# Kernel optimization log

Hardware: AMD Instinct MI355X
Metric: run time of the kernel (lower is better)

The kernel has to match this reference:

```python
import jax, jax.numpy as jnp
import numpy as np

_SQRT1_2 = 0.7071067811865476

B, S, D, N, NCH = 4, 2048, 1024, 32768, 8


def setup_inputs() -> dict:
    key = jax.random.key(0)
    ks = jax.random.split(key, 6)
    return {
        "x": jax.random.normal(ks[0], (B, S, D), jnp.float32),
        "h": jax.random.normal(ks[1], (B, S, D), jnp.float32),
        "emb": jax.random.normal(ks[2], (N, D), jnp.float32),
        "tau_offset": jax.random.normal(ks[3], (B, S, 1), jnp.float32),
        "w_read": jax.random.normal(ks[4], (N, D), jnp.float32),
        "w_write": jax.random.normal(ks[5], (N, D), jnp.float32),
        "n_chunks": NCH,
    }


def _srw_chunked(x, h, emb_unit, tau_offset, w_read, w_write, n_chunks):
    b, s, d = x.shape
    n = emb_unit.shape[0]
    cs = n // n_chunks
    h_bf = h.astype(jnp.bfloat16)
    x_bf = x.astype(jnp.bfloat16)
    emb_bf = emb_unit.astype(jnp.bfloat16)
    read_bf = w_read.astype(jnp.bfloat16)
    write_bf = w_write.astype(jnp.bfloat16)
    z1 = jnp.zeros((b, s, 1), jnp.float32)

    # ---- pass 1: online score statistics over chunks of N ----
    @jax.checkpoint
    def stats_step(carry, i):
        s_sum, sq_sum, cube_sum, ns_sum, ns_sq = carry
        ec = jax.lax.dynamic_slice_in_dim(emb_bf, i * cs, cs, axis=0)
        sc = (h_bf @ ec.T).astype(jnp.float32)  # [B,S,cs]
        s_sum = s_sum + sc.sum(-1, keepdims=True)
        sq_sum = sq_sum + (sc ** 2).sum(-1, keepdims=True)
        cube_sum = cube_sum + (sc ** 3).sum(-1, keepdims=True)
        pns = sc.mean(axis=(0, 1))  # per-neuron mean score [cs]
        return ((s_sum, sq_sum, cube_sum, ns_sum + pns.sum(), ns_sq + (pns ** 2).sum()), None)

    (s_sum, sq_sum, cube_sum, ns_sum, ns_sq), _ = jax.lax.scan(
        stats_step, (z1, z1, z1, jnp.float32(0.0), jnp.float32(0.0)), jnp.arange(n_chunks))

    s_mean = s_sum / n
    s_std = jnp.sqrt(sq_sum / n - s_mean ** 2) + 1e-08
    tau = s_mean + tau_offset * s_std
    cube_mean = cube_sum / n
    central_third = cube_mean - 3.0 * s_mean * s_std ** 2 - s_mean ** 3
    score_skew = jax.lax.stop_gradient((central_third / (s_std ** 3 + 1e-08)).mean())
    mean_score = ns_sum / n
    var_score = ns_sq / n - mean_score ** 2
    score_lb = var_score / (mean_score ** 2 + var_score + 0.01)

    # ---- pass 2: erf-threshold gate + read/write GEMM accumulate ----
    @jax.checkpoint
    def gate_step(carry, i):
        out, wcost, gmax, act, strong, phib, zsum, z075c, z030c, glg = carry
        s0 = i * cs
        ec = jax.lax.dynamic_slice_in_dim(emb_bf, s0, cs, axis=0)
        rc = jax.lax.dynamic_slice_in_dim(read_bf, s0, cs, axis=0)
        wc = jax.lax.dynamic_slice_in_dim(write_bf, s0, cs, axis=0)
        rc = rc / (jnp.linalg.norm(rc, axis=-1, keepdims=True) + 1e-08)
        wc = wc / (jnp.linalg.norm(wc, axis=-1, keepdims=True) + 1e-08)
        z = ((h_bf @ ec.T).astype(jnp.float32) - tau) / s_std  # [B,S,cs]
        phi = 0.5 * (1.0 + jax.lax.erf(z * _SQRT1_2))
        gate = jnp.where(z > 0, z * phi, 0.0)
        xr = x_bf @ rc.T  # [B,S,cs]
        c_out = ((gate.astype(jnp.bfloat16) * xr) @ wc).astype(jnp.float32)  # [B,S,D]
        g_safe = gate + 1e-08
        new = (
            out + c_out,
            wcost + gate.sum(-1, keepdims=True),
            jnp.maximum(gmax, gate.max(-1, keepdims=True)),
            act + (gate > 0.0).astype(jnp.float32).sum(-1, keepdims=True),
            strong + (gate > 0.5).astype(jnp.float32).sum(-1, keepdims=True),
            phib + ((phi > 0.95) | (phi < 0.05)).astype(jnp.float32).sum(-1, keepdims=True),
            zsum + jnp.where(z > 0, z, 0.0).sum(-1, keepdims=True),
            z075c + ((z > 0) & (z < 0.75)).astype(jnp.float32).sum(-1, keepdims=True),
            z030c + ((z > 0) & (z < 0.3)).astype(jnp.float32).sum(-1, keepdims=True),
            glg + (gate * jnp.log(g_safe)).sum(-1, keepdims=True),
        )
        return (new, None)

    init = (jnp.zeros((b, s, d), jnp.float32), z1, jnp.full((b, s, 1), -1e9, jnp.float32),
            z1, z1, z1, z1, z1, z1, z1)
    (raw_out, wcost, gmax, act, strong, phib, zsum, z075c, z030c, glg), _ = jax.lax.scan(
        gate_step, init, jnp.arange(n_chunks))

    den = jnp.maximum(wcost, 1.0)
    out = (raw_out / den).astype(jnp.bfloat16)
    score_std_out = s_std.mean()
    es_out = wcost.mean()
    active_n_mean = act.mean()
    z_mean_active = zsum / (act + 1e-08)
    active_eps = act + 1e-08
    z_lt_075_frac = jax.lax.stop_gradient((z075c / active_eps).mean())
    z_lt_030_frac = jax.lax.stop_gradient((z030c / active_eps).mean())
    tau_abs_mean = jax.lax.stop_gradient(tau).mean()
    active_per_token_std = jax.lax.stop_gradient(act).std()
    gate_sum_eps = wcost + 1e-08
    entropy_per_token = -glg / gate_sum_eps + jnp.log(gate_sum_eps)
    gate_entropy = jax.lax.stop_gradient(entropy_per_token).mean()
    return (out.astype(jnp.float32), act / n, gmax, score_lb, score_std_out, es_out,
            active_n_mean, strong / n, phib / n, z_mean_active, tau_abs_mean,
            z_lt_075_frac, z_lt_030_frac, score_skew, active_per_token_std, gate_entropy)


def reference(x, h, emb, tau_offset, w_read, w_write, n_chunks):
    emb_unit = emb / (jnp.linalg.norm(emb, axis=-1, keepdims=True) + 1e-08)
    return _srw_chunked(x, h, emb_unit, tau_offset, w_read, w_write, n_chunks)
```

## Files before the change

### kernel.cpp

```cpp
#include <hip/hip_runtime.h>

#define DEV __device__ __forceinline__

typedef __attribute__((ext_vector_type(4))) float f32x4;
typedef __attribute__((ext_vector_type(8))) short s16x8;
typedef __attribute__((ext_vector_type(8))) unsigned short u16x8;

static const int NTOK = 8192;
static const int DD   = 1024;
static const int NNEU = 32768;
static const int NC   = 8192;

static const int OUT_ACT    = 8388608;
static const int OUT_GMAX   = 8396800;
static const int OUT_SLB    = 8404992;
static const int OUT_SSTD   = 8404993;
static const int OUT_ES     = 8404994;
static const int OUT_ANM    = 8404995;
static const int OUT_STRONG = 8404996;
static const int OUT_PHIB   = 8413188;
static const int OUT_ZMEAN  = 8421380;
static const int OUT_TAUM   = 8429572;
static const int OUT_Z75    = 8429573;
static const int OUT_Z30    = 8429574;
static const int OUT_SKEW   = 8429575;
static const int OUT_ASTD   = 8429576;
static const int OUT_ENT    = 8429577;

DEV unsigned short f2bf(float f){
  unsigned u = __float_as_uint(f);
  u += 0x7fffu + ((u >> 16) & 1u);
  return (unsigned short)(u >> 16);
}
DEV float bf2f(unsigned short h){ return __uint_as_float(((unsigned)h) << 16); }
DEV float rnd_bf(float f){ return bf2f(f2bf(f)); }

template<int AUX>
DEV void gl_lds16(const void* g, void* l){
  __builtin_amdgcn_global_load_lds(
      (const __attribute__((address_space(1))) unsigned int*)g,
      (__attribute__((address_space(3))) unsigned int*)l, 16, 0, AUX);
}

DEV f32x4 mfma16(s16x8 a, s16x8 b, f32x4 c){
  return __builtin_amdgcn_mfma_f32_16x16x32_bf16(a, b, c, 0, 0, 0);
}

template<int AUX>
DEV void stage4(const unsigned short* __restrict__ G, size_t ld, int k0,
                unsigned short* L, int t){
  #pragma unroll
  for (int i = 0; i < 4; i++){
    int ch = i*256 + t;
    int row = ch >> 3, c = ch & 7;
    int cs = c ^ (row & 7);
    int wb = (i*256 + (t & 192)) * 16;
    gl_lds16<AUX>(G + (size_t)row * ld + k0 + cs*8, (char*)L + wb);
  }
}

DEV s16x8 frg(const unsigned short* L, int R, int kk, int lq){
  int cc = ((kk >> 3) + lq) ^ (R & 7);
  return *(const s16x8*)((const char*)L + R*128 + cc*16);
}

DEV void waitv_bar(){
  asm volatile("s_waitcnt vmcnt(0)" ::: "memory");
  __builtin_amdgcn_s_barrier();
  __builtin_amdgcn_sched_barrier(0);
}

DEV int2 xcd64(){
  int orig = blockIdx.y * 64 + blockIdx.x;
  int xcd = orig & 7, p = orig >> 3;
  int sqy = p >> 6, off = p & 63;
  int2 r;
  r.x = xcd*8 + (off & 7);
  r.y = sqy*8 + (off >> 3);
  return r;
}


__global__ __launch_bounds__(256) void k_norms(const float* __restrict__ e,
    const float* __restrict__ r_, const float* __restrict__ w_,
    float* __restrict__ inv_e, float* __restrict__ inv_r, float* __restrict__ inv_w){
  int t = threadIdx.x, l = t & 63, wv = t >> 6;
  int row = blockIdx.x * 4 + wv;
  const float4* ep = (const float4*)(e  + (size_t)row * DD);
  const float4* rp = (const float4*)(r_ + (size_t)row * DD);
  const float4* wp = (const float4*)(w_ + (size_t)row * DD);
  float se = 0.f, sr = 0.f, sw = 0.f;
  #pragma unroll
  for (int j = 0; j < 4; j++){
    float4 v = ep[j*64 + l];
    se += v.x*v.x + v.y*v.y + v.z*v.z + v.w*v.w;
    float4 a = rp[j*64 + l];
    float a0 = rnd_bf(a.x), a1 = rnd_bf(a.y), a2 = rnd_bf(a.z), a3 = rnd_bf(a.w);
    sr += a0*a0 + a1*a1 + a2*a2 + a3*a3;
    float4 c = wp[j*64 + l];
    float c0 = rnd_bf(c.x), c1 = rnd_bf(c.y), c2 = rnd_bf(c.z), c3 = rnd_bf(c.w);
    sw += c0*c0 + c1*c1 + c2*c2 + c3*c3;
  }
  #pragma unroll
  for (int d = 1; d < 64; d <<= 1){
    se += __shfl_xor(se, d); sr += __shfl_xor(sr, d); sw += __shfl_xor(sw, d);
  }
  if (l == 0){
    inv_e[row] = 1.f / (sqrtf(se) + 1e-8f);
    inv_r[row] = 1.f / (sqrtf(sr) + 1e-8f);
    inv_w[row] = 1.f / (sqrtf(sw) + 1e-8f);
  }
}

__global__ __launch_bounds__(256) void k_cast_scale(const float* __restrict__ in,
    const float* __restrict__ inv, unsigned short* __restrict__ o, int round_first){
  size_t i = (size_t)blockIdx.x * 256 + threadIdx.x;
  int row = (int)(i >> 8);
  float s = inv[row];
  float4 v = ((const float4*)in)[i];
  ushort4 r;
  if (round_first){
    r.x = f2bf(rnd_bf(v.x) * s); r.y = f2bf(rnd_bf(v.y) * s);
    r.z = f2bf(rnd_bf(v.z) * s); r.w = f2bf(rnd_bf(v.w) * s);
  } else {
    r.x = f2bf(v.x * s); r.y = f2bf(v.y * s);
    r.z = f2bf(v.z * s); r.w = f2bf(v.w * s);
  }
  ((ushort4*)o)[i] = r;
}

__global__ __launch_bounds__(256) void k_cast(const float* __restrict__ in,
                                              unsigned short* __restrict__ o){
  size_t i = (size_t)blockIdx.x * 256 + threadIdx.x;
  float4 v = ((const float4*)in)[i];
  ushort4 r;
  r.x = f2bf(v.x); r.y = f2bf(v.y); r.z = f2bf(v.z); r.w = f2bf(v.w);
  ((ushort4*)o)[i] = r;
}

__global__ __launch_bounds__(256) void k_wcnT(const float* __restrict__ w_,
    const float* __restrict__ invw, unsigned short* __restrict__ o){
  __shared__ unsigned short tile[64][65];
  int t = threadIdx.x;
  int n0b = blockIdx.x * 64, d0 = blockIdx.y * 64;
  #pragma unroll
  for (int i = 0; i < 16; i++){
    int idx = t + i*256;
    int r = idx >> 6, c = idx & 63;
    float v = w_[(size_t)(n0b + r) * DD + d0 + c];
    tile[c][r] = f2bf(rnd_bf(v) * invw[n0b + r]);
  }
  __syncthreads();
  #pragma unroll
  for (int i = 0; i < 16; i++){
    int idx = t + i*256;
    int rd = idx >> 6, cn = idx & 63;
    o[(size_t)(d0 + rd) * NNEU + n0b + cn] = tile[rd][cn];
  }
}

__global__ __launch_bounds__(256) void k_hsum(const unsigned short* __restrict__ hb,
                                              float* __restrict__ hs){
  int t = threadIdx.x; int r0 = blockIdx.x * 128;
  float s[4] = {0.f, 0.f, 0.f, 0.f};
  for (int r = 0; r < 128; r++){
    const unsigned short* row = hb + (size_t)(r0 + r) * DD;
    #pragma unroll
    for (int j = 0; j < 4; j++) s[j] += bf2f(row[j*256 + t]);
  }
  #pragma unroll
  for (int j = 0; j < 4; j++) atomicAdd(hs + j*256 + t, s[j]);
}

__global__ __launch_bounds__(256) void k_pns(const unsigned short* __restrict__ eb,
    const float* __restrict__ hs, float* __restrict__ ns){
  __shared__ float hsh[1024];
  __shared__ float pr[8];
  int t = threadIdx.x, l = t & 63, wv = t >> 6;
  for (int i = t; i < 1024; i += 256) hsh[i] = hs[i];
  __syncthreads();
  float bs = 0.f, bq = 0.f;
  for (int it = 0; it < 32; it++){
    int row = blockIdx.x * 128 + it*4 + wv;
    const unsigned short* er = eb + (size_t)row * DD + l*16;
    float s = 0.f;
    #pragma unroll
    for (int j = 0; j < 16; j++) s += hsh[l*16 + j] * bf2f(er[j]);
    #pragma unroll
    for (int d = 1; d < 64; d <<= 1) s += __shfl_xor(s, d);
    float pns = s * (1.f / 8192.f);
    bs += pns; bq += pns * pns;
  }
  if (l == 0){ pr[wv*2] = bs; pr[wv*2 + 1] = bq; }
  __syncthreads();
  if (t == 0){
    atomicAdd(ns + 0, pr[0] + pr[2] + pr[4] + pr[6]);
    atomicAdd(ns + 1, pr[1] + pr[3] + pr[5] + pr[7]);
  }
}


template<bool DO_STATS>
__global__ __launch_bounds__(256, 2) void k_score(
    const unsigned short* __restrict__ A, const unsigned short* __restrict__ Bm,
    float* __restrict__ s_sum, float* __restrict__ sq_sum, float* __restrict__ cu_sum,
    unsigned short* __restrict__ Sout, int do_store)
{
  __shared__ unsigned short lds[32768];
  const int t = threadIdx.x, l = t & 63, wv = t >> 6;
  const int wm = wv >> 1, wn = wv & 1;
  const int lq = l >> 4, lr = l & 15;
  int2 rm = xcd64();
  const int bx = rm.x, by = rm.y;
  const unsigned short* Ab = A  + (size_t)by * 128 * DD;
  const unsigned short* Bb = Bm + (size_t)bx * 128 * DD;
  f32x4 acc[4][4];
  #pragma unroll
  for (int m = 0; m < 4; m++)
    #pragma unroll
    for (int n = 0; n < 4; n++) acc[m][n] = (f32x4){0.f, 0.f, 0.f, 0.f};

  stage4<0>(Ab, DD, 0, lds, t);
  stage4<0>(Bb, DD, 0, lds + 8192, t);
  waitv_bar();
  int cur = 0;
  for (int ks = 0; ks < 16; ++ks){
    unsigned short* Lc = lds + cur*16384;
    if (ks + 1 < 16){
      unsigned short* Ln = lds + (cur^1)*16384;
      int k0 = (ks+1)*64;
      stage4<0>(Ab, DD, k0, Ln, t);
      stage4<0>(Bb, DD, k0, Ln + 8192, t);
    }
    #pragma unroll
    for (int kk = 0; kk < 64; kk += 32){
      s16x8 af[4], bf4[4];
      #pragma unroll
      for (int m = 0; m < 4; m++) af[m]  = frg(Lc, wm*64 + m*16 + lr, kk, lq);
      #pragma unroll
      for (int n = 0; n < 4; n++) bf4[n] = frg(Lc + 8192, wn*64 + n*16 + lr, kk, lq);
      #pragma unroll
      for (int m = 0; m < 4; m++)
        #pragma unroll
        for (int n = 0; n < 4; n++)
          acc[m][n] = mfma16(af[m], bf4[n], acc[m][n]);
    }
    waitv_bar();
    cur ^= 1;
  }

  unsigned short* sl = lds;
  float* red = (float*)((char*)lds + 49152);

  if (do_store){
    #pragma unroll
    for (int m = 0; m < 4; m++)
    #pragma unroll
    for (int n = 0; n < 4; n++)
    #pragma unroll
    for (int r = 0; r < 4; r++){
      int rl = wm*64 + m*16 + lq*4 + r;
      int cl = wn*64 + n*16 + lr;
      sl[rl*136 + cl] = f2bf(acc[m][n][r]);
    }
  }
  if (DO_STATS){
    #pragma unroll
    for (int m = 0; m < 4; m++)
    #pragma unroll
    for (int r = 0; r < 4; r++){
      float s1 = 0.f, s2 = 0.f, s3 = 0.f;
      #pragma unroll
      for (int n = 0; n < 4; n++){
        float v = rnd_bf(acc[m][n][r]);
        s1 += v; float v2 = v*v; s2 += v2; s3 += v2*v;
      }
      #pragma unroll
      for (int d = 1; d < 16; d <<= 1){
        s1 += __shfl_xor(s1, d); s2 += __shfl_xor(s2, d); s3 += __shfl_xor(s3, d);
      }
      if (lr == 0){
        int rl = wm*64 + m*16 + lq*4 + r;
        float* p = red + (wn*128 + rl)*4;
        p[0] = s1; p[1] = s2; p[2] = s3;
      }
    }
  }
  __syncthreads();
  if (do_store){
    #pragma unroll
    for (int i = 0; i < 8; i++){
      int idx = i*2048 + t*8;
      int row = idx >> 7, col = idx & 127;
      u16x8 v = *(const u16x8*)&sl[row*136 + col];
      *(u16x8*)(Sout + (size_t)(by*128 + row) * NC + bx*128 + col) = v;
    }
  }
  if (DO_STATS){
    const int row0 = by * 128;
    for (int idx = t; idx < 384; idx += 256){
      int rl = idx / 3, st = idx - rl*3;
      float v = red[rl*4 + st] + red[(128 + rl)*4 + st];
      float* dst = (st == 0) ? s_sum : (st == 1) ? sq_sum : cu_sum;
      atomicAdd(dst + row0 + rl, v);
    }
  }
}

__global__ __launch_bounds__(256) void k_tau(const float* __restrict__ s_sum,
    const float* __restrict__ sq_sum, const float* __restrict__ tof,
    float* __restrict__ tau, float* __restrict__ rstd){
  int i = blockIdx.x * 256 + threadIdx.x;
  float mean = s_sum[i] * (1.f / 32768.f);
  float var  = sq_sum[i] * (1.f / 32768.f) - mean*mean;
  float sstd = sqrtf(fmaxf(var, 0.f)) + 1e-8f;
  tau[i]  = mean + tof[i] * sstd;
  rstd[i] = 1.f / sstd;
}


__global__ __launch_bounds__(256, 2) void k_gateS(
    const unsigned short* __restrict__ Xb, const unsigned short* __restrict__ Rb,
    const float* __restrict__ tau, const float* __restrict__ rstd,
    unsigned short* __restrict__ SP, int n0,
    float* __restrict__ wcostp, float* __restrict__ gmaxp, float* __restrict__ actp,
    float* __restrict__ strongp, float* __restrict__ phibp, float* __restrict__ zsump,
    float* __restrict__ z075p, float* __restrict__ z030p, float* __restrict__ glgp)
{
  __shared__ unsigned short lds[32768];
  const int t = threadIdx.x, l = t & 63, wv = t >> 6;
  const int wm = wv >> 1, wn = wv & 1;
  const int lq = l >> 4, lr = l & 15;
  int2 rm = xcd64();
  const int bx = rm.x, by = rm.y;
  const unsigned short* Xp = Xb + (size_t)by * 128 * DD;
  const unsigned short* Rp = Rb + (size_t)(n0 + bx*128) * DD;
  f32x4 accX[4][4];
  #pragma unroll
  for (int m = 0; m < 4; m++)
    #pragma unroll
    for (int n = 0; n < 4; n++) accX[m][n] = (f32x4){0.f,0.f,0.f,0.f};

  stage4<0>(Xp, DD, 0, lds, t);
  stage4<0>(Rp, DD, 0, lds + 8192, t);
  waitv_bar();
  int cur = 0;
  for (int ks = 0; ks < 16; ++ks){
    unsigned short* Lc = lds + cur*16384;
    if (ks + 1 < 16){
      unsigned short* Ln = lds + (cur^1)*16384;
      int k0 = (ks+1)*64;
      stage4<0>(Xp, DD, k0, Ln, t);
      stage4<0>(Rp, DD, k0, Ln + 8192, t);
    }
    #pragma unroll
    for (int kk = 0; kk < 64; kk += 32){
      s16x8 af[4], bf4[4];
      #pragma unroll
      for (int m = 0; m < 4; m++) af[m]  = frg(Lc, wm*64 + m*16 + lr, kk, lq);
      #pragma unroll
      for (int n = 0; n < 4; n++) bf4[n] = frg(Lc + 8192, wn*64 + n*16 + lr, kk, lq);
      #pragma unroll
      for (int m = 0; m < 4; m++)
        #pragma unroll
        for (int n = 0; n < 4; n++)
          accX[m][n] = mfma16(af[m], bf4[n], accX[m][n]);
    }
    waitv_bar();
    cur ^= 1;
  }

  unsigned short sv[4][4][4];
  #pragma unroll
  for (int m = 0; m < 4; m++)
  #pragma unroll
  for (int r = 0; r < 4; r++)
  #pragma unroll
  for (int n = 0; n < 4; n++){
    int gr = by*128 + wm*64 + m*16 + lq*4 + r;
    int gc = bx*128 + wn*64 + n*16 + lr;
    sv[m][r][n] = SP[(size_t)gr * NC + gc];
  }

  unsigned short* plds = lds;
  float* red = (float*)((char*)lds + 49152);

  #pragma unroll
  for (int m = 0; m < 4; m++)
  #pragma unroll
  for (int r = 0; r < 4; r++){
    int rl = wm*64 + m*16 + lq*4 + r;
    int gr = by*128 + rl;
    float tauv = tau[gr], rs = rstd[gr];
    float wsum = 0.f, gmx = 0.f, ac = 0.f, stc = 0.f, pb = 0.f;
    float zs = 0.f, z7 = 0.f, z3 = 0.f, gl = 0.f;
    #pragma unroll
    for (int n = 0; n < 4; n++){
      float sc = bf2f(sv[m][r][n]);
      float xr = rnd_bf(accX[m][n][r]);
      float z = (sc - tauv) * rs;
      float phi = 0.5f * (1.0f + erff(z * 0.70710678118654752440f));
      float gate = (z > 0.f) ? z * phi : 0.f;
      wsum += gate; gmx = fmaxf(gmx, gate);
      if (gate > 0.f)  ac  += 1.f;
      if (gate > 0.5f) stc += 1.f;
      if (phi > 0.95f || phi < 0.05f) pb += 1.f;
      if (z > 0.f){ zs += z; if (z < 0.75f) z7 += 1.f; if (z < 0.3f) z3 += 1.f; }
      gl += gate * __logf(gate + 1e-8f);
      float p = rnd_bf(gate) * xr;
      plds[rl*136 + wn*64 + n*16 + lr] = f2bf(p);
    }
    #pragma unroll
    for (int d = 1; d < 16; d <<= 1){
      wsum += __shfl_xor(wsum, d); gmx = fmaxf(gmx, __shfl_xor(gmx, d));
      ac += __shfl_xor(ac, d);  stc += __shfl_xor(stc, d); pb += __shfl_xor(pb, d);
      zs += __shfl_xor(zs, d);  z7  += __shfl_xor(z7, d);  z3 += __shfl_xor(z3, d);
      gl += __shfl_xor(gl, d);
    }
    if (lr == 0){
      float* p = red + (wn*128 + rl)*10;
      p[0]=wsum; p[1]=gmx; p[2]=ac; p[3]=stc; p[4]=pb; p[5]=zs; p[6]=z7; p[7]=z3; p[8]=gl;
    }
  }
  __syncthreads();
  #pragma unroll
  for (int i = 0; i < 8; i++){
    int idx = i*2048 + t*8;
    int row = idx >> 7, col = idx & 127;
    u16x8 v = *(const u16x8*)&plds[row*136 + col];
    *(u16x8*)(SP + (size_t)(by*128 + row) * NC + bx*128 + col) = v;
  }
  for (int idx = t; idx < 1152; idx += 256){
    int rl = idx / 9, st = idx - rl*9;
    float a = red[rl*10 + st], b = red[(128 + rl)*10 + st];
    int gr = by*128 + rl;
    if (st == 1){
      atomicMax((int*)(gmaxp + gr), __float_as_int(fmaxf(a, b)));
    } else {
      float v = a + b;
      float* dst = (st==0)?wcostp:(st==2)?actp:(st==3)?strongp:(st==4)?phibp:
                   (st==5)?zsump:(st==6)?z075p:(st==7)?z030p:glgp;
      atomicAdd(dst + gr, v);
    }
  }
}


__global__ __launch_bounds__(256, 2) void k_out_gemm(
    const unsigned short* __restrict__ Pm, const unsigned short* __restrict__ Bt,
    float* __restrict__ outp, const float* __restrict__ wcost, int accum, int fin)
{
  __shared__ unsigned short lds[32768];
  const int t = threadIdx.x, l = t & 63, wv = t >> 6;
  const int wm = wv >> 1, wn = wv & 1;
  const int lq = l >> 4, lr = l & 15;
  const int bx = blockIdx.x, by = blockIdx.y;
  const unsigned short* Ab = Pm + (size_t)by * 128 * NC;
  const unsigned short* Bb = Bt + (size_t)bx * 128 * NNEU;
  f32x4 acc[4][4];
  #pragma unroll
  for (int m = 0; m < 4; m++)
    #pragma unroll
    for (int n = 0; n < 4; n++) acc[m][n] = (f32x4){0.f,0.f,0.f,0.f};

  const int NT = NC / 64;
  stage4<2>(Ab, NC, 0, lds, t);
  stage4<0>(Bb, NNEU, 0, lds + 8192, t);
  waitv_bar();
  int cur = 0;
  for (int ks = 0; ks < NT; ++ks){
    unsigned short* Lc = lds + cur*16384;
    if (ks + 1 < NT){
      unsigned short* Ln = lds + (cur^1)*16384;
      int k0 = (ks+1)*64;
      stage4<2>(Ab, NC, k0, Ln, t);
      stage4<0>(Bb, NNEU, k0, Ln + 8192, t);
    }
    #pragma unroll
    for (int kk = 0; kk < 64; kk += 32){
      s16x8 af[4], bf4[4];
      #pragma unroll
      for (int m = 0; m < 4; m++) af[m]  = frg(Lc, wm*64 + m*16 + lr, kk, lq);
      #pragma unroll
      for (int n = 0; n < 4; n++) bf4[n] = frg(Lc + 8192, wn*64 + n*16 + lr, kk, lq);
      #pragma unroll
      for (int m = 0; m < 4; m++)
        #pragma unroll
        for (int n = 0; n < 4; n++)
          acc[m][n] = mfma16(af[m], bf4[n], acc[m][n]);
    }
    waitv_bar();
    cur ^= 1;
  }
  #pragma unroll
  for (int m = 0; m < 4; m++)
  #pragma unroll
  for (int r = 0; r < 4; r++){
    int gr = by*128 + wm*64 + m*16 + lq*4 + r;
    float den = fin ? fmaxf(wcost[gr], 1.f) : 1.f;
    #pragma unroll
    for (int n = 0; n < 4; n++){
      int dc = bx*128 + wn*64 + n*16 + lr;
      float* o = outp + (size_t)gr * DD + dc;
      float v = acc[m][n][r];
      if (accum) v += *o;
      if (fin)   v = rnd_bf(v / den);
      *o = v;
    }
  }
}


__global__ __launch_bounds__(1024) void k_final(
    const float* __restrict__ s_sum, const float* __restrict__ sq_sum,
    const float* __restrict__ cu_sum, const float* __restrict__ tof,
    const float* __restrict__ wcost, const float* __restrict__ gmax,
    const float* __restrict__ act, const float* __restrict__ strong,
    const float* __restrict__ phib, const float* __restrict__ zsum,
    const float* __restrict__ z075, const float* __restrict__ z030,
    const float* __restrict__ glg, const float* __restrict__ ns,
    float* __restrict__ out)
{
  int tid = threadIdx.x;
  float s0=0,s1=0,s2=0,s3=0,s4=0,s5=0,s6=0,s7=0,s8=0;
  for (int i = tid; i < NTOK; i += 1024){
    float mean = s_sum[i] * (1.f / 32768.f);
    float var  = sq_sum[i] * (1.f / 32768.f) - mean*mean;
    float sstd = sqrtf(fmaxf(var, 0.f)) + 1e-8f;
    float tauv = mean + tof[i] * sstd;
    float wc = wcost[i], ac = act[i];
    out[OUT_ACT + i]    = ac * (1.f / 32768.f);
    out[OUT_GMAX + i]   = gmax[i];
    out[OUT_STRONG + i] = strong[i] * (1.f / 32768.f);
    out[OUT_PHIB + i]   = phib[i] * (1.f / 32768.f);
    out[OUT_ZMEAN + i]  = zsum[i] / (ac + 1e-8f);
    float c3 = cu_sum[i] * (1.f / 32768.f) - 3.f*mean*sstd*sstd - mean*mean*mean;
    float skew = c3 / (sstd*sstd*sstd + 1e-8f);
    float gse = wc + 1e-8f;
    float ent = -glg[i] / gse + logf(gse);
    s0 += sstd; s1 += wc; s2 += ac; s3 += ac*ac; s4 += tauv;
    s5 += z075[i] / (ac + 1e-8f); s6 += z030[i] / (ac + 1e-8f); s7 += skew; s8 += ent;
  }
  __shared__ float rb[16][9];
  int lane = tid & 63, wid = tid >> 6;
  #pragma unroll
  for (int d = 1; d < 64; d <<= 1){
    s0 += __shfl_xor(s0,d); s1 += __shfl_xor(s1,d); s2 += __shfl_xor(s2,d);
    s3 += __shfl_xor(s3,d); s4 += __shfl_xor(s4,d); s5 += __shfl_xor(s5,d);
    s6 += __shfl_xor(s6,d); s7 += __shfl_xor(s7,d); s8 += __shfl_xor(s8,d);
  }
  if (lane == 0){
    rb[wid][0]=s0; rb[wid][1]=s1; rb[wid][2]=s2; rb[wid][3]=s3; rb[wid][4]=s4;
    rb[wid][5]=s5; rb[wid][6]=s6; rb[wid][7]=s7; rb[wid][8]=s8;
  }
  __syncthreads();
  if (tid == 0){
    float S[9];
    for (int k = 0; k < 9; k++){ float a = 0.f; for (int w2 = 0; w2 < 16; w2++) a += rb[w2][k]; S[k] = a; }
    const float inv = 1.f / 8192.f;
    float act_mean = S[2] * inv;
    out[OUT_SSTD] = S[0] * inv;
    out[OUT_ES]   = S[1] * inv;
    out[OUT_ANM]  = act_mean;
    out[OUT_ASTD] = sqrtf(fmaxf(S[3]*inv - act_mean*act_mean, 0.f));
    out[OUT_TAUM] = S[4] * inv;
    out[OUT_Z75]  = S[5] * inv;
    out[OUT_Z30]  = S[6] * inv;
    out[OUT_SKEW] = S[7] * inv;
    out[OUT_ENT]  = S[8] * inv;
    float ms = ns[0] * (1.f / 32768.f);
    float vs = ns[1] * (1.f / 32768.f) - ms*ms;
    out[OUT_SLB] = vs / (ms*ms + vs + 0.01f);
  }
}


extern "C" void kernel_launch(void* const* d_in, const int* in_sizes, int n_in,
                              void* d_out, int out_size, void* d_ws, size_t ws_size,
                              hipStream_t stream)
{
  (void)in_sizes; (void)n_in; (void)out_size;
  const float* x   = (const float*)d_in[0];
  const float* h   = (const float*)d_in[1];
  const float* emb = (const float*)d_in[2];
  const float* tof = (const float*)d_in[3];
  const float* wr  = (const float*)d_in[4];
  const float* ww  = (const float*)d_in[5];
  float* out = (float*)d_out;
  char* ws = (char*)d_ws;

  size_t off = 0;
  auto get = [&](size_t n){ size_t o = off; off += (n + 255) & ~(size_t)255; return o; };
  unsigned short* rcn_bf = (unsigned short*)(ws + get((size_t)NNEU*DD*2));
  unsigned short* emb_bf = (unsigned short*)(ws + get((size_t)NNEU*DD*2));
  unsigned short* wcnT   = (unsigned short*)(ws + get((size_t)DD*NNEU*2));
  unsigned short* h_bf   = (unsigned short*)(ws + get((size_t)NTOK*DD*2));
  unsigned short* x_bf   = (unsigned short*)(ws + get((size_t)NTOK*DD*2));
  float* inv_e = (float*)(ws + get(NNEU*4));
  float* inv_r = (float*)(ws + get(NNEU*4));
  float* inv_w = (float*)(ws + get(NNEU*4));
  size_t zoff = off;
  float* hsum   = (float*)(ws + get(DD*4));
  float* s_sum  = (float*)(ws + get(NTOK*4));
  float* sq_sum = (float*)(ws + get(NTOK*4));
  float* cu_sum = (float*)(ws + get(NTOK*4));
  float* tau    = (float*)(ws + get(NTOK*4));
  float* rstd   = (float*)(ws + get(NTOK*4));
  float* wcost  = (float*)(ws + get(NTOK*4));
  float* gmax   = (float*)(ws + get(NTOK*4));
  float* act    = (float*)(ws + get(NTOK*4));
  float* strong = (float*)(ws + get(NTOK*4));
  float* phib   = (float*)(ws + get(NTOK*4));
  float* zsum   = (float*)(ws + get(NTOK*4));
  float* z075   = (float*)(ws + get(NTOK*4));
  float* z030   = (float*)(ws + get(NTOK*4));
  float* glg    = (float*)(ws + get(NTOK*4));
  float* ns     = (float*)(ws + get(256));
  size_t zlen = off - zoff;

  const size_t szS = (size_t)NTOK * NC * 2;
  size_t poff = (off + 4095) & ~(size_t)4095;
  size_t avail = ws_size > poff ? ws_size - poff : 0;
  int kst = (int)(avail / szS);
  if (kst > 4) kst = 4;
  if (kst < 1) kst = 1;
  unsigned short* Sb = (unsigned short*)(ws + poff);

  hipMemsetAsync(ws + zoff, 0, zlen, stream);

  dim3 b256(256);
  dim3 gC(64, 64);
  k_norms<<<dim3(NNEU/4), b256, 0, stream>>>(emb, wr, ww, inv_e, inv_r, inv_w);
  k_cast_scale<<<dim3(NNEU*DD/4/256), b256, 0, stream>>>(emb, inv_e, emb_bf, 0);
  k_cast_scale<<<dim3(NNEU*DD/4/256), b256, 0, stream>>>(wr, inv_r, rcn_bf, 1);
  k_cast<<<dim3(NTOK*DD/4/256), b256, 0, stream>>>(h, h_bf);
  k_cast<<<dim3(NTOK*DD/4/256), b256, 0, stream>>>(x, x_bf);
  k_hsum<<<dim3(NTOK/128), b256, 0, stream>>>(h_bf, hsum);
  k_pns<<<dim3(NNEU/128), b256, 0, stream>>>(emb_bf, hsum, ns);

  for (int c = 0; c < 4; ++c){
    unsigned short* slot = Sb + (size_t)(c < kst ? c : 0) * NTOK * NC;
    k_score<true><<<gC, b256, 0, stream>>>(h_bf, emb_bf + (size_t)c*NC*DD,
        s_sum, sq_sum, cu_sum, slot, c < kst ? 1 : 0);
  }
  k_tau<<<dim3(NTOK/256), b256, 0, stream>>>(s_sum, sq_sum, tof, tau, rstd);
  k_wcnT<<<dim3(NNEU/64, DD/64), b256, 0, stream>>>(ww, inv_w, wcnT);

  for (int c = 0; c < 4; ++c){
    int slot_i = (c < kst) ? c : (c % kst);
    unsigned short* slot = Sb + (size_t)slot_i * NTOK * NC;
    if (c >= kst){
      k_score<false><<<gC, b256, 0, stream>>>(h_bf, emb_bf + (size_t)c*NC*DD,
          nullptr, nullptr, nullptr, slot, 1);
    }
    k_gateS<<<gC, b256, 0, stream>>>(x_bf, rcn_bf, tau, rstd, slot, c*NC,
        wcost, gmax, act, strong, phib, zsum, z075, z030, glg);
    k_out_gemm<<<dim3(DD/128, NTOK/128), b256, 0, stream>>>(slot, wcnT + (size_t)c*NC,
        out, wcost, c > 0 ? 1 : 0, c == 3 ? 1 : 0);
  }
  k_final<<<dim3(1), dim3(1024), 0, stream>>>(s_sum, sq_sum, cu_sum, tof, wcost, gmax,
      act, strong, phib, zsum, z075, z030, glg, ns, out);
}
```

Baseline: 4.649 ms.

## Restructure GEMM epilogues to row-per-thread-pair with vectorized score loads

Both the score GEMM epilogue and the gate GEMM epilogue now stage the accumulator tile through LDS first. Afterwards each pair of threads owns one row and processes 64 contiguous columns per thread. In the gate kernel this replaces scattered 2-byte global reads of the score matrix with 16-byte vector loads and stores, and removes the 16-lane shuffle reductions and the second LDS reduction pass. The stats reduction is likewise folded into the row-wise pass, with the statistics now computed from the bf16 values read back from LDS. The cost is an extra barrier before the elementwise work and more per-thread serial work per row.

```diff
diff --git a/kernel.cpp b/kernel.cpp
--- a/kernel.cpp
+++ b/kernel.cpp
@@ -250,59 +250,41 @@
   }
 
   unsigned short* sl = lds;
-  float* red = (float*)((char*)lds + 49152);
-
-  if (do_store){
-    #pragma unroll
-    for (int m = 0; m < 4; m++)
-    #pragma unroll
-    for (int n = 0; n < 4; n++)
-    #pragma unroll
-    for (int r = 0; r < 4; r++){
-      int rl = wm*64 + m*16 + lq*4 + r;
-      int cl = wn*64 + n*16 + lr;
-      sl[rl*136 + cl] = f2bf(acc[m][n][r]);
+  #pragma unroll
+  for (int m = 0; m < 4; m++)
+  #pragma unroll
+  for (int n = 0; n < 4; n++)
+  #pragma unroll
+  for (int r = 0; r < 4; r++){
+    int rl = wm*64 + m*16 + lq*4 + r;
+    int cl = wn*64 + n*16 + lr;
+    sl[rl*136 + cl] = f2bf(acc[m][n][r]);
+  }
+  __syncthreads();
+
+  int row = t >> 1, half = t & 1;
+  const unsigned short* sp = &sl[row*136 + half*64];
+  unsigned short* Sdst = Sout + (size_t)(by*128 + row) * NC + bx*128 + half*64;
+  float s1 = 0.f, s2 = 0.f, s3 = 0.f;
+  #pragma unroll
+  for (int j = 0; j < 8; j++){
+    u16x8 v = *(const u16x8*)(sp + j*8);
+    if (do_store) *(u16x8*)(Sdst + j*8) = v;
+    if (DO_STATS){
+      #pragma unroll
+      for (int e = 0; e < 8; e++){
+        float f = bf2f(v[e]);
+        s1 += f; float f2 = f*f; s2 += f2; s3 += f2*f;
+      }
     }
   }
   if (DO_STATS){
-    #pragma unroll
-    for (int m = 0; m < 4; m++)
-    #pragma unroll
-    for (int r = 0; r < 4; r++){
-      float s1 = 0.f, s2 = 0.f, s3 = 0.f;
-      #pragma unroll
-      for (int n = 0; n < 4; n++){
-        float v = rnd_bf(acc[m][n][r]);
-        s1 += v; float v2 = v*v; s2 += v2; s3 += v2*v;
-      }
-      #pragma unroll
-      for (int d = 1; d < 16; d <<= 1){
-        s1 += __shfl_xor(s1, d); s2 += __shfl_xor(s2, d); s3 += __shfl_xor(s3, d);
-      }
-      if (lr == 0){
-        int rl = wm*64 + m*16 + lq*4 + r;
-        float* p = red + (wn*128 + rl)*4;
-        p[0] = s1; p[1] = s2; p[2] = s3;
-      }
-    }
-  }
-  __syncthreads();
-  if (do_store){
-    #pragma unroll
-    for (int i = 0; i < 8; i++){
-      int idx = i*2048 + t*8;
-      int row = idx >> 7, col = idx & 127;
-      u16x8 v = *(const u16x8*)&sl[row*136 + col];
-      *(u16x8*)(Sout + (size_t)(by*128 + row) * NC + bx*128 + col) = v;
-    }
-  }
-  if (DO_STATS){
-    const int row0 = by * 128;
-    for (int idx = t; idx < 384; idx += 256){
-      int rl = idx / 3, st = idx - rl*3;
-      float v = red[rl*4 + st] + red[(128 + rl)*4 + st];
-      float* dst = (st == 0) ? s_sum : (st == 1) ? sq_sum : cu_sum;
-      atomicAdd(dst + row0 + rl, v);
+    s1 += __shfl_xor(s1, 1); s2 += __shfl_xor(s2, 1); s3 += __shfl_xor(s3, 1);
+    if (half == 0){
+      int gr = by*128 + row;
+      atomicAdd(s_sum + gr, s1);
+      atomicAdd(sq_sum + gr, s2);
+      atomicAdd(cu_sum + gr, s3);
     }
   }
 }
@@ -370,34 +352,34 @@
     cur ^= 1;
   }
 
-  unsigned short sv[4][4][4];
+  unsigned short* plds = lds;
   #pragma unroll
   for (int m = 0; m < 4; m++)
   #pragma unroll
-  for (int r = 0; r < 4; r++)
-  #pragma unroll
-  for (int n = 0; n < 4; n++){
-    int gr = by*128 + wm*64 + m*16 + lq*4 + r;
-    int gc = bx*128 + wn*64 + n*16 + lr;
-    sv[m][r][n] = SP[(size_t)gr * NC + gc];
-  }
-
-  unsigned short* plds = lds;
-  float* red = (float*)((char*)lds + 49152);
-
-  #pragma unroll
-  for (int m = 0; m < 4; m++)
+  for (int n = 0; n < 4; n++)
   #pragma unroll
   for (int r = 0; r < 4; r++){
     int rl = wm*64 + m*16 + lq*4 + r;
-    int gr = by*128 + rl;
-    float tauv = tau[gr], rs = rstd[gr];
-    float wsum = 0.f, gmx = 0.f, ac = 0.f, stc = 0.f, pb = 0.f;
-    float zs = 0.f, z7 = 0.f, z3 = 0.f, gl = 0.f;
-    #pragma unroll
-    for (int n = 0; n < 4; n++){
-      float sc = bf2f(sv[m][r][n]);
-      float xr = rnd_bf(accX[m][n][r]);
+    int cl = wn*64 + n*16 + lr;
+    plds[rl*136 + cl] = f2bf(accX[m][n][r]);
+  }
+  __syncthreads();
+
+  int row = t >> 1, half = t & 1;
+  int gr = by*128 + row;
+  float tauv = tau[gr], rs = rstd[gr];
+  unsigned short* Srow = SP + (size_t)gr * NC + bx*128 + half*64;
+  const unsigned short* xrp = &plds[row*136 + half*64];
+  float wsum = 0.f, gmx = 0.f, ac = 0.f, stc = 0.f, pb = 0.f;
+  float zs = 0.f, z7 = 0.f, z3 = 0.f, gl = 0.f;
+  #pragma unroll
+  for (int j = 0; j < 8; j++){
+    u16x8 sv8 = *(const u16x8*)(Srow + j*8);
+    u16x8 pv;
+    #pragma unroll
+    for (int e = 0; e < 8; e++){
+      float sc = bf2f(sv8[e]);
+      float xr = bf2f(xrp[j*8 + e]);
       float z = (sc - tauv) * rs;
       float phi = 0.5f * (1.0f + erff(z * 0.70710678118654752440f));
       float gate = (z > 0.f) ? z * phi : 0.f;
@@ -407,41 +389,25 @@
       if (phi > 0.95f || phi < 0.05f) pb += 1.f;
       if (z > 0.f){ zs += z; if (z < 0.75f) z7 += 1.f; if (z < 0.3f) z3 += 1.f; }
       gl += gate * __logf(gate + 1e-8f);
-      float p = rnd_bf(gate) * xr;
-      plds[rl*136 + wn*64 + n*16 + lr] = f2bf(p);
-    }
-    #pragma unroll
-    for (int d = 1; d < 16; d <<= 1){
-      wsum += __shfl_xor(wsum, d); gmx = fmaxf(gmx, __shfl_xor(gmx, d));
-      ac += __shfl_xor(ac, d);  stc += __shfl_xor(stc, d); pb += __shfl_xor(pb, d);
-      zs += __shfl_xor(zs, d);  z7  += __shfl_xor(z7, d);  z3 += __shfl_xor(z3, d);
-      gl += __shfl_xor(gl, d);
-    }
-    if (lr == 0){
-      float* p = red + (wn*128 + rl)*10;
-      p[0]=wsum; p[1]=gmx; p[2]=ac; p[3]=stc; p[4]=pb; p[5]=zs; p[6]=z7; p[7]=z3; p[8]=gl;
-    }
-  }
-  __syncthreads();
-  #pragma unroll
-  for (int i = 0; i < 8; i++){
-    int idx = i*2048 + t*8;
-    int row = idx >> 7, col = idx & 127;
-    u16x8 v = *(const u16x8*)&plds[row*136 + col];
-    *(u16x8*)(SP + (size_t)(by*128 + row) * NC + bx*128 + col) = v;
-  }
-  for (int idx = t; idx < 1152; idx += 256){
-    int rl = idx / 9, st = idx - rl*9;
-    float a = red[rl*10 + st], b = red[(128 + rl)*10 + st];
-    int gr = by*128 + rl;
-    if (st == 1){
-      atomicMax((int*)(gmaxp + gr), __float_as_int(fmaxf(a, b)));
-    } else {
-      float v = a + b;
-      float* dst = (st==0)?wcostp:(st==2)?actp:(st==3)?strongp:(st==4)?phibp:
-                   (st==5)?zsump:(st==6)?z075p:(st==7)?z030p:glgp;
-      atomicAdd(dst + gr, v);
-    }
+      pv[e] = f2bf(rnd_bf(gate) * xr);
+    }
+    *(u16x8*)(Srow + j*8) = pv;
+  }
+  wsum += __shfl_xor(wsum, 1); gmx = fmaxf(gmx, __shfl_xor(gmx, 1));
+  ac   += __shfl_xor(ac, 1);   stc += __shfl_xor(stc, 1);
+  pb   += __shfl_xor(pb, 1);   zs  += __shfl_xor(zs, 1);
+  z7   += __shfl_xor(z7, 1);   z3  += __shfl_xor(z3, 1);
+  gl   += __shfl_xor(gl, 1);
+  if (half == 0){
+    atomicAdd(wcostp + gr, wsum);
+    atomicMax((int*)(gmaxp + gr), __float_as_int(gmx));
+    atomicAdd(actp + gr, ac);
+    atomicAdd(strongp + gr, stc);
+    atomicAdd(phibp + gr, pb);
+    atomicAdd(zsump + gr, zs);
+    atomicAdd(z075p + gr, z7);
+    atomicAdd(z030p + gr, z3);
+    atomicAdd(glgp + gr, gl);
   }
 }
 
```

After: 3.777 ms. 1.23x faster.
